# Kernel tuning notes

Measured on AMD Instinct MI355X. Metric: run time of the kernel, lower is better.

The kernel has to match this reference:

```python
import jax, jax.numpy as jnp
import numpy as np
import math

B, N, H, NH, L, NC = 8, 128, 128, 4, 4, 1
DH = H // NH
EPS = 1e-5

def _gelu(x):
    return jax.nn.gelu(x, approximate=False)  # torch nn.GELU default is exact erf

def _ln(x, g, b):
    m = x.mean(-1, keepdims=True)
    v = ((x - m) ** 2).mean(-1, keepdims=True)
    return (x - m) / jnp.sqrt(v + EPS) * g + b

def _bn(x, mask, g, b):
    # BatchNorm1d over valid (unpadded) nodes only, batch statistics (train mode)
    m = mask[..., None].astype(x.dtype)
    cnt = m.sum()
    mu = (x * m).sum((0, 1)) / cnt
    var = (((x - mu) ** 2) * m).sum((0, 1)) / cnt
    return (x - mu) / jnp.sqrt(var + EPS) * g + b

def _forward(e, u, atom_emb, bond_emb, eigw_W, eigw_b, mha_norm_g, mha_norm_b, qkv_W, qkv_b, out_W, out_b, ffn_norm_g, ffn_norm_b, ffn1_W, ffn1_b, ffn2_W, ffn2_b, dec_W, dec_b, fe1_W, fe1_b, fe2_W, fe2_b, pre_W, pre_b, f1_W, f1_b, bn1_g, bn1_b, f2_W, f2_b, bn2_g, bn2_b, lin_W, lin_b, node_feat, edge_feat, length):
    Bx, Nx = e.shape
    node_mask = jnp.arange(Nx)[None, :] < length[:, None]                        # [B,N]
    edge_mask = (node_mask[:, :, None] & node_mask[:, None, :]).astype(e.dtype)  # [B,src,dst]
    # SineEncoding
    div = jnp.exp(jnp.arange(0, H, 2, dtype=e.dtype) * (-math.log(10000.0) / H))
    pe = (e * 100.0)[:, :, None] * div
    eeig = jnp.concatenate([e[..., None], jnp.sin(pe), jnp.cos(pe)], axis=-1)    # [B,N,H+1]
    eig = eeig @ eigw_W.T + eigw_b                                               # [B,N,H]
    # multi-head self-attention over eigenvalue tokens with key padding mask
    xm = _ln(eig, mha_norm_g, mha_norm_b)
    qkv = xm @ qkv_W.T + qkv_b
    q, k, v = jnp.split(qkv, 3, axis=-1)
    q = q.reshape(Bx, Nx, NH, DH).transpose(0, 2, 1, 3)
    k = k.reshape(Bx, Nx, NH, DH).transpose(0, 2, 1, 3)
    v = v.reshape(Bx, Nx, NH, DH).transpose(0, 2, 1, 3)
    scores = jnp.einsum('bhqd,bhkd->bhqk', q, k) / math.sqrt(DH)
    scores = jnp.where(node_mask[:, None, None, :], scores, -jnp.inf)
    attn = jax.nn.softmax(scores, axis=-1)                                       # [B,NH,N,N]
    ctx = jnp.einsum('bhqk,bhkd->bhqd', attn, v).transpose(0, 2, 1, 3).reshape(Bx, Nx, H)
    eig = eig + (ctx @ out_W.T + out_b)
    y = _ln(eig, ffn_norm_g, ffn_norm_b)
    y = _gelu(y @ ffn1_W.T + ffn1_b) @ ffn2_W.T + ffn2_b
    eig = eig + y
    new_e = (eig @ dec_W.T + dec_b).transpose(0, 2, 1)                           # [B,NH,N]
    # spectral bases: identity + u @ diag(new_e_k) @ u^T per head, as fused diagonal scale
    filters = jnp.einsum('bnm,bkm,bpm->bnpk', u, new_e, u)                       # [B,N,N,NH]
    eye = jnp.broadcast_to(jnp.eye(Nx, dtype=e.dtype)[None, :, :, None], (Bx, Nx, Nx, 1))
    bases = jnp.concatenate([eye, filters], axis=-1)                             # [B,N,N,NH+1]
    bases = _gelu(_gelu(bases @ fe1_W.T + fe1_b) @ fe2_W.T + fe2_b)              # [B,N,N,H]
    xf = atom_emb[node_feat]                                                     # [B,N,H]
    ea = bond_emb[edge_feat]                                                     # [B,N,N,H]
    for l in range(L):
        # copy_u gather + per-edge FFN * bases + masked scatter-sum to dst
        msg = _gelu((xf[:, :, None, :] + ea) @ pre_W[l].T + pre_b[l]) * bases
        aggr = jnp.einsum('bijh,bij->bjh', msg, edge_mask)
        xf = xf + aggr
        y = xf @ f1_W[l].T + f1_b[l]
        y = jax.nn.relu(_bn(y, node_mask, bn1_g[l], bn1_b[l]))
        y = y @ f2_W[l].T + f2_b[l]
        y = jax.nn.relu(_bn(y, node_mask, bn2_g[l], bn2_b[l]))
        xf = xf + y
    nm = node_mask[..., None].astype(e.dtype)
    h = (xf * nm).sum(1) / length[:, None].astype(e.dtype)                       # AvgPooling over valid nodes
    h = h @ lin_W.T + lin_b
    return h, new_e, attn

def setup_inputs():
    key = jax.random.key(0)
    ks = iter(jax.random.split(key, 64))
    def w(*shape):
        return jax.random.normal(next(ks), shape, dtype=jnp.float32) * 0.02
    z = lambda *s: jnp.zeros(s, dtype=jnp.float32)
    o = lambda *s: jnp.ones(s, dtype=jnp.float32)
    e = jax.random.uniform(next(ks), (B, N), dtype=jnp.float32) * 2.0
    u = jnp.linalg.qr(jax.random.normal(next(ks), (B, N, N), dtype=jnp.float32))[0]
    inp = {
        'e': e, 'u': u,
        'atom_emb': w(40, H), 'bond_emb': w(10, H).at[0].set(0.0),
        'eigw_W': w(H, H + 1), 'eigw_b': z(H),
        'mha_norm_g': o(H), 'mha_norm_b': z(H),
        'qkv_W': w(3 * H, H), 'qkv_b': z(3 * H),
        'out_W': w(H, H), 'out_b': z(H),
        'ffn_norm_g': o(H), 'ffn_norm_b': z(H),
        'ffn1_W': w(H, H), 'ffn1_b': z(H),
        'ffn2_W': w(H, H), 'ffn2_b': z(H),
        'dec_W': w(NH, H), 'dec_b': z(NH),
        'fe1_W': w(H, NH + 1), 'fe1_b': z(H),
        'fe2_W': w(H, H), 'fe2_b': z(H),
        'pre_W': w(L, H, H), 'pre_b': z(L, H),
        'f1_W': w(L, H, H), 'f1_b': z(L, H),
        'bn1_g': o(L, H), 'bn1_b': z(L, H),
        'f2_W': w(L, H, H), 'f2_b': z(L, H),
        'bn2_g': o(L, H), 'bn2_b': z(L, H),
        'lin_W': w(NC, H), 'lin_b': z(NC),
        'node_feat': jax.random.randint(next(ks), (B, N), 0, 40),
        'edge_feat': jax.random.randint(next(ks), (B, N, N), 0, 10),
        'length': 64 + jax.random.randint(next(ks), (B,), 0, N - 63),
    }
    return inp

def reference(e, u, atom_emb, bond_emb, eigw_W, eigw_b, mha_norm_g, mha_norm_b, qkv_W, qkv_b, out_W, out_b, ffn_norm_g, ffn_norm_b, ffn1_W, ffn1_b, ffn2_W, ffn2_b, dec_W, dec_b, fe1_W, fe1_b, fe2_W, fe2_b, pre_W, pre_b, f1_W, f1_b, bn1_g, bn1_b, f2_W, f2_b, bn2_g, bn2_b, lin_W, lin_b, node_feat, edge_feat, length):
    return _forward(e, u, atom_emb, bond_emb, eigw_W, eigw_b, mha_norm_g, mha_norm_b, qkv_W, qkv_b, out_W, out_b, ffn_norm_g, ffn_norm_b, ffn1_W, ffn1_b, ffn2_W, ffn2_b, dec_W, dec_b, fe1_W, fe1_b, fe2_W, fe2_b, pre_W, pre_b, f1_W, f1_b, bn1_g, bn1_b, f2_W, f2_b, bn2_g, bn2_b, lin_W, lin_b, node_feat, edge_feat, length)
```

## Files before the change

kernel.cpp:

```cpp
#include <hip/hip_runtime.h>
#include <hip/hip_bf16.h>
#include <math.h>

#define BB 8
#define NN 128
#define HH 128
#define NHD 4
#define DHD 32
#define LAY 4
#define EPSV 1e-5f

typedef __hip_bfloat16 bf16;
typedef unsigned short ushortt;
typedef short bf16x8 __attribute__((ext_vector_type(8)));
typedef float f32x4 __attribute__((ext_vector_type(4)));

__device__ __forceinline__ float b2f(bf16 x){ return __bfloat162float(x); }
__device__ __forceinline__ bf16 f2b(float x){ return __float2bfloat16(x); }
__device__ __forceinline__ float us2f(ushortt u){ return __uint_as_float(((unsigned)u)<<16); }
__device__ __forceinline__ ushortt f2us(float x){ bf16 b=__float2bfloat16(x); return *(ushortt*)&b; }
__device__ __forceinline__ float gelu_f(float x){ return 0.5f*x*(1.0f+erff(x*0.7071067811865476f)); }
__device__ __forceinline__ float gelu_h(float x){
  float t = 0.7978845608028654f*x*(1.0f + 0.044715f*x*x);
  float e = __expf(2.0f*t);
  float th = 1.0f - 2.0f/(e + 1.0f);
  return 0.5f*x*(1.0f + th);
}
__device__ __forceinline__ float erf_fast(float x){
  float ax = fabsf(x);
  float t = __builtin_amdgcn_rcpf(__builtin_fmaf(0.3275911f, ax, 1.0f));
  float p = __builtin_fmaf(1.061405429f, t, -1.453152027f);
  p = __builtin_fmaf(p, t, 1.421413741f);
  p = __builtin_fmaf(p, t, -0.284496736f);
  p = __builtin_fmaf(p, t, 0.254829592f);
  p = p*t;
  float e = __expf(-ax*ax);
  float y = __builtin_fmaf(-p, e, 1.0f);
  return __builtin_copysignf(y, x);
}
__device__ __forceinline__ float gelu_fe(float x){
  return 0.5f*x*(1.0f + erf_fast(x*0.7071067811865476f));
}


__global__ __launch_bounds__(256) void k_prep(const float* __restrict__ fe2W,
    const float* __restrict__ preW, const float* __restrict__ eigW,
    const float* __restrict__ qkvW, const float* __restrict__ outW,
    const float* __restrict__ ffn1W, const float* __restrict__ ffn2W,
    const float* __restrict__ f1W, const float* __restrict__ f2W,
    const float* __restrict__ aemb, const int* __restrict__ nf,
    const float* __restrict__ bemb, const float* __restrict__ preb,
    ushortt* __restrict__ wbf, float* __restrict__ gs, float* __restrict__ xf0,
    float* __restrict__ eigWT, float* __restrict__ qkvWT, float* __restrict__ outWT,
    float* __restrict__ ffn1WT, float* __restrict__ ffn2WT,
    float* __restrict__ f1WT, float* __restrict__ f2WT,
    float* __restrict__ bondWall){
  int idx = blockIdx.x*256 + threadIdx.x;
  if (idx < 10240) gs[idx] = 0.f;
  if (idx < 81920){
    float v = (idx < 16384) ? fe2W[idx] : preW[idx - 16384];
    wbf[idx] = f2us(v);
  }
  if (idx < 131072){
    int node = idx >> 7, h2 = idx & 127;
    xf0[idx] = aemb[nf[node]*HH + h2];
  }
  if (idx < 16512){ int o = idx/129, kq = idx - o*129; eigWT[kq*128+o] = eigW[idx]; }
  if (idx < 49152){ int o = idx>>7, m = idx&127; qkvWT[m*384+o] = qkvW[idx]; }
  if (idx < 16384){ int o = idx>>7, m = idx&127;
    outWT[m*128+o]  = outW[idx];
    ffn1WT[m*128+o] = ffn1W[idx];
    ffn2WT[m*128+o] = ffn2W[idx];
  }
  if (idx < 65536){ int l = idx>>14, r = idx&16383; int o = r>>7, m = r&127;
    f1WT[l*16384 + m*128+o] = f1W[idx];
    f2WT[l*16384 + m*128+o] = f2W[idx];
  }
  if (idx < 5120){
    int l = idx / 1280; int r = idx - l*1280; int e2 = r >> 7; int hcol = r & 127;
    const float* br = bemb + e2*128;
    const float* wr = preW + l*16384 + hcol*128;
    float acc = preb[l*128 + hcol];
    for (int m=0;m<128;m++) acc += br[m]*wr[m];
    bondWall[idx] = acc;
  }
}


__global__ void k_fe_a(const float* __restrict__ e, const float* __restrict__ eigWT,
                       const float* __restrict__ eigb, const float* __restrict__ g,
                       const float* __restrict__ bt, const float* __restrict__ qkvWT,
                       const float* __restrict__ qkvb,
                       float* __restrict__ eigout, float* __restrict__ q,
                       float* __restrict__ kT, float* __restrict__ v){
  int row = blockIdx.x; int tid = threadIdx.x;
  int b = row >> 7, n = row & 127;
  __shared__ float ee[129]; __shared__ float buf[128]; __shared__ float xm[128];
  float ev = e[row];
  if (tid < 64){
    float dv = expf(-0.1439115683121279f * (float)tid);
    float pe = ev * 100.0f * dv;
    ee[1+tid] = sinf(pe);
    ee[65+tid] = cosf(pe);
  }
  if (tid == 0) ee[0] = ev;
  __syncthreads();
  float x = eigb[tid];
  for (int k2=0;k2<129;k2++) x += ee[k2]*eigWT[k2*128+tid];
  eigout[row*HH+tid] = x;
  buf[tid]=x; __syncthreads();
  for (int s2=64;s2>0;s2>>=1){ if(tid<s2) buf[tid]+=buf[tid+s2]; __syncthreads(); }
  float mean = buf[0]*(1.0f/128.0f); __syncthreads();
  float d = x-mean; buf[tid]=d*d; __syncthreads();
  for (int s2=64;s2>0;s2>>=1){ if(tid<s2) buf[tid]+=buf[tid+s2]; __syncthreads(); }
  float var = buf[0]*(1.0f/128.0f);
  xm[tid] = d*rsqrtf(var+EPSV)*g[tid]+bt[tid];
  __syncthreads();
  #pragma unroll
  for (int s3=0;s3<3;s3++){
    float acc = qkvb[s3*HH+tid];
    const float* wt = qkvWT + s3*HH + tid;
    for (int m=0;m<HH;m++) acc += xm[m]*wt[m*384];
    if (s3==0) q[row*HH+tid]=acc;
    else if (s3==1) kT[b*16384 + tid*128 + n]=acc;
    else v[row*HH+tid]=acc;
  }
}

__global__ void k_attn(const float* __restrict__ q, const float* __restrict__ kT,
                       const int* __restrict__ length,
                       float* __restrict__ attnf, float* __restrict__ outp){
  int bx = blockIdx.x;
  int qi = bx & 127, hd = (bx>>7)&3, b = bx>>9;
  int tid = threadIdx.x;
  int len = length[b];
  __shared__ float qv[DHD]; __shared__ float red[128];
  if (tid < DHD) qv[tid] = q[(b*NN+qi)*HH + hd*DHD + tid];
  __syncthreads();
  float s = -1e30f;
  if (tid < len){
    const float* kr = kT + b*16384 + hd*DHD*128 + tid;
    float sc=0.f;
    for (int d2=0; d2<DHD; d2++) sc += qv[d2]*kr[d2*128];
    s = sc * 0.17677669529663687f;
  }
  red[tid]=s; __syncthreads();
  for (int st=64;st>0;st>>=1){ if(tid<st) red[tid]=fmaxf(red[tid],red[tid+st]); __syncthreads(); }
  float mx = red[0]; __syncthreads();
  float p = (tid<len)? expf(s-mx):0.0f;
  red[tid]=p; __syncthreads();
  for (int st=64;st>0;st>>=1){ if(tid<st) red[tid]+=red[tid+st]; __syncthreads(); }
  float a = p / red[0];
  int idx = ((b*NHD+hd)*NN+qi)*NN+tid;
  attnf[idx]=a;
  outp[4104 + idx]=a;
}

__global__ void k_fe_c(const float* __restrict__ attnf, const float* __restrict__ v,
                       const float* __restrict__ outWT, const float* __restrict__ outb,
                       const float* __restrict__ fng, const float* __restrict__ fnb,
                       const float* __restrict__ w1T, const float* __restrict__ b1,
                       const float* __restrict__ w2T, const float* __restrict__ b2,
                       float* __restrict__ eig){
  int row = blockIdx.x; int b = row>>7, qi = row&127;
  int tid = threadIdx.x;
  __shared__ float c[128]; __shared__ float buf[128]; __shared__ float xm[128]; __shared__ float tt[128];
  int hd = tid>>5;
  const float* ar = attnf + ((b*NHD+hd)*NN+qi)*NN;
  float acc=0.f;
  for (int j=0;j<NN;j++) acc += ar[j]*v[(b*NN+j)*HH+tid];
  c[tid]=acc; __syncthreads();
  float o = outb[tid];
  for (int m=0;m<HH;m++) o += c[m]*outWT[m*128+tid];
  float x = eig[row*HH+tid] + o;
  buf[tid]=x; __syncthreads();
  for (int s2=64;s2>0;s2>>=1){ if(tid<s2) buf[tid]+=buf[tid+s2]; __syncthreads(); }
  float mean=buf[0]*(1.f/128.f); __syncthreads();
  float d=x-mean; buf[tid]=d*d; __syncthreads();
  for (int s2=64;s2>0;s2>>=1){ if(tid<s2) buf[tid]+=buf[tid+s2]; __syncthreads(); }
  float var=buf[0]*(1.f/128.f);
  xm[tid]=d*rsqrtf(var+EPSV)*fng[tid]+fnb[tid];
  __syncthreads();
  float a1=b1[tid];
  for (int m=0;m<HH;m++) a1+=xm[m]*w1T[m*128+tid];
  tt[tid]=gelu_f(a1); __syncthreads();
  float a2=b2[tid];
  for (int m=0;m<HH;m++) a2+=tt[m]*w2T[m*128+tid];
  eig[row*HH+tid]=x+a2;
}

__global__ void k_dec(const float* __restrict__ eig, const float* dW, const float* db,
                      float* __restrict__ newe, float* __restrict__ outp){
  int b = blockIdx.x, n = threadIdx.x;
  __shared__ float w[NHD*HH];
  for (int i=n;i<NHD*HH;i+=128) w[i]=dW[i];
  __syncthreads();
  float acc[NHD];
  #pragma unroll
  for (int kk=0;kk<NHD;kk++) acc[kk]=db[kk];
  const float* er = eig + (b*NN+n)*HH;
  for (int h2=0;h2<HH;h2++){
    float ev = er[h2];
    #pragma unroll
    for (int kk=0;kk<NHD;kk++) acc[kk]+=ev*w[kk*HH+h2];
  }
  #pragma unroll
  for (int kk=0;kk<NHD;kk++){
    int idx=(b*NHD+kk)*NN+n; newe[idx]=acc[kk];
    outp[8 + idx]=acc[kk];
  }
}


__global__ void k_filters(const float* __restrict__ u, const float* __restrict__ newe,
                          const int* __restrict__ length, float* __restrict__ filt){
  int b = blockIdx.x, n0 = blockIdx.y*16, p0 = blockIdx.z*16;
  int len = length[b];
  if (n0 >= len || p0 >= len) return;
  int tx = threadIdx.x, ty = threadIdx.y; int tid = ty*16+tx;
  __shared__ float un[16][17], upt[16][17], wk[4][16];
  float acc[4]={0.f,0.f,0.f,0.f};
  for (int mt=0; mt<8; mt++){
    __syncthreads();
    un[ty][tx]  = u[(b*NN+n0+ty)*NN + mt*16+tx];
    upt[tx][ty] = u[(b*NN+p0+ty)*NN + mt*16+tx];
    if (tid<64) wk[tid>>4][tid&15] = newe[(b*NHD+(tid>>4))*NN + mt*16 + (tid&15)];
    __syncthreads();
    #pragma unroll
    for (int mm=0;mm<16;mm++){
      float pr = un[ty][mm]*upt[mm][tx];
      #pragma unroll
      for (int kk=0;kk<4;kk++) acc[kk] += pr*wk[kk][mm];
    }
  }
  float4 o; o.x=acc[0];o.y=acc[1];o.z=acc[2];o.w=acc[3];
  *(float4*)&filt[((b*NN+n0+ty)*NN+p0+tx)*4] = o;
}

__global__ __launch_bounds__(256) void k_fe2(const float* __restrict__ filt,
    const float* __restrict__ w1g, const float* __restrict__ b1g,
    const ushortt* __restrict__ w2bf, const float* __restrict__ b2g,
    const int* __restrict__ length,
    bf16* __restrict__ bases){
  int blk = blockIdx.x;
  int bi = blk >> 1;
  int r0 = (blk & 1)*64;
  int b = bi >> 7;
  int nloc = bi & 127;
  int len = length[b];
  if (nloc >= len || r0 >= len) return;
  int tid = threadIdx.x;
  int lane = tid & 63, w = tid >> 6, quad = lane >> 4, l15 = lane & 15;
  int pr = r0 + w*16 + l15;
  float4 f4 = ((const float4*)filt)[bi*128 + pr];
  __shared__ alignas(16) ushortt sW2[128*136];
  __shared__ float w1p[128*8];
  __shared__ float b2s[128];
  for (int idx = tid; idx < 2048; idx += 256){
    int r = idx >> 4, cb = idx & 15;
    *(uint4*)&sW2[r*136 + cb*8] = *(const uint4*)&w2bf[r*128 + cb*8];
  }
  for (int idx = tid; idx < 1024; idx += 256){
    int r = idx >> 3, c = idx & 7;
    w1p[idx] = (c==0) ? b1g[r] : (c<=5 ? w1g[r*5 + c-1] : 0.f);
  }
  if (tid < 128) b2s[tid] = b2g[tid];
  __syncthreads();
  bool wact = (r0 + w*16) < len;
  f32x4 acc[8];
  #pragma unroll
  for (int nt=0;nt<8;nt++) acc[nt] = (f32x4){0.f,0.f,0.f,0.f};
  if (wact){
    float dg = (pr == nloc) ? 1.0f : 0.0f;
    for (int kk = 0; kk < 128; kk += 32){
      bf16x8 af;
      #pragma unroll
      for (int j=0;j<8;j++){
        int m = kk + quad*8 + j;
        const float4 wa = *(const float4*)&w1p[m*8];
        const float2 wb = *(const float2*)&w1p[m*8+4];
        float a = wa.x + wa.y*dg + wa.z*f4.x + wa.w*f4.y + wb.x*f4.z + wb.y*f4.w;
        af[j] = (short)f2us(gelu_fe(a));
      }
      #pragma unroll
      for (int nt=0;nt<8;nt++){
        bf16x8 bfr = *(const bf16x8*)&sW2[(nt*16+l15)*136 + kk + quad*8];
        acc[nt] = __builtin_amdgcn_mfma_f32_16x16x32_bf16(af, bfr, acc[nt], 0, 0, 0);
      }
    }
  }
  __syncthreads();
  ushortt* sT = sW2;
  if (wact){
    #pragma unroll
    for (int nt=0;nt<8;nt++){
      int h = nt*16 + l15;
      float bb = b2s[h];
      #pragma unroll
      for (int reg=0;reg<4;reg++){
        int lr = w*16 + quad*4 + reg;
        sT[lr*132 + h] = f2us(gelu_fe(acc[nt][reg] + bb));
      }
    }
  }
  __syncthreads();
  int rmax = len - r0; if (rmax > 64) rmax = 64;
  ushort4* gout = (ushort4*)(bases + (size_t)bi*16384 + r0*128);
  for (int idx = tid; idx < rmax*32; idx += 256){
    int row = idx >> 5, seg = idx & 31;
    gout[idx] = *(const ushort4*)&sT[row*132 + seg*4];
  }
}


__global__ __launch_bounds__(256) void k_xwl2(const float* __restrict__ xfprev,
    const float* __restrict__ t2, const float* __restrict__ gsum2p,
    const float* __restrict__ gsq2p, const float* __restrict__ g2p,
    const float* __restrict__ bb2p, const int* __restrict__ length, int prevapply,
    const ushortt* __restrict__ wbfl, float* __restrict__ xfB,
    float* __restrict__ xfW){
  int blk = blockIdx.x;
  int b = blk >> 2, rq = blk & 3;
  int tid = threadIdx.x;
  int lane = tid & 63, w = tid >> 6, quad = lane >> 4, l15 = lane & 15;
  __shared__ alignas(16) ushortt sA[32*136];
  __shared__ float smu[128], sistd[128], sg[128], sbb[128];
  if (prevapply && tid < 128){
    float cnt = 0.f;
    for (int q2=0;q2<BB;q2++) cnt += (float)length[q2];
    float mu = gsum2p[tid]/cnt;
    float var = gsq2p[tid]/cnt - mu*mu;
    smu[tid]=mu; sistd[tid]=rsqrtf(fmaxf(var,0.0f)+EPSV);
    sg[tid]=g2p[tid]; sbb[tid]=bb2p[tid];
  }
  __syncthreads();
  for (int idx = tid; idx < 1024; idx += 256){
    int r = idx >> 5, c = idx & 31;
    int gr = b*128 + rq*32 + r;
    float4 xv = ((const float4*)xfprev)[gr*32 + c];
    if (prevapply){
      float4 tv = ((const float4*)t2)[gr*32 + c];
      int f0 = c*4;
      xv.x += fmaxf((tv.x-smu[f0+0])*sistd[f0+0]*sg[f0+0]+sbb[f0+0], 0.f);
      xv.y += fmaxf((tv.y-smu[f0+1])*sistd[f0+1]*sg[f0+1]+sbb[f0+1], 0.f);
      xv.z += fmaxf((tv.z-smu[f0+2])*sistd[f0+2]*sg[f0+2]+sbb[f0+2], 0.f);
      xv.w += fmaxf((tv.w-smu[f0+3])*sistd[f0+3]*sg[f0+3]+sbb[f0+3], 0.f);
      ((float4*)xfB)[gr*32 + c] = xv;
    }
    ushort4 o;
    o.x=f2us(xv.x); o.y=f2us(xv.y); o.z=f2us(xv.z); o.w=f2us(xv.w);
    *(ushort4*)&sA[r*136 + c*4] = o;
  }
  __syncthreads();
  f32x4 acc[2][2];
  #pragma unroll
  for (int mt=0;mt<2;mt++)
    #pragma unroll
    for (int nt=0;nt<2;nt++) acc[mt][nt] = (f32x4){0.f,0.f,0.f,0.f};
  #pragma unroll
  for (int kk = 0; kk < 128; kk += 32){
    bf16x8 af[2], bfr[2];
    #pragma unroll
    for (int mt=0;mt<2;mt++) af[mt] = *(const bf16x8*)&sA[(mt*16+l15)*136 + kk + quad*8];
    #pragma unroll
    for (int nt=0;nt<2;nt++) bfr[nt] = *(const bf16x8*)&wbfl[((w*2+nt)*16+l15)*128 + kk + quad*8];
    #pragma unroll
    for (int mt=0;mt<2;mt++)
      #pragma unroll
      for (int nt=0;nt<2;nt++)
        acc[mt][nt] = __builtin_amdgcn_mfma_f32_16x16x32_bf16(af[mt], bfr[nt], acc[mt][nt], 0, 0, 0);
  }
  #pragma unroll
  for (int mt=0;mt<2;mt++)
    #pragma unroll
    for (int nt=0;nt<2;nt++){
      int h = (w*2+nt)*16 + l15;
      #pragma unroll
      for (int reg=0;reg<4;reg++){
        int prr = rq*32 + mt*16 + quad*4 + reg;
        xfW[(b*128 + prr)*128 + h] = acc[mt][nt][reg];
      }
    }
}

__global__ __launch_bounds__(512) void k_edge(const float* __restrict__ xfin, float* __restrict__ xfout,
    const bf16* __restrict__ bases, const float* __restrict__ xfW,
    const float* __restrict__ bondWl, const int* __restrict__ ef,
    const int* __restrict__ length,
    const float* __restrict__ w1t, const float* __restrict__ bias1,
    float* __restrict__ t1, float* __restrict__ gst){
  int bj = blockIdx.x; int b = bj >> 7, j = bj & 127;
  int len = length[b];
  int tid = threadIdx.x; int h = tid & 127, ih = tid >> 7;
  __shared__ float sBW[10][128];
  __shared__ int sEf[128];
  __shared__ float part[4][128];
  for (int idx = tid; idx < 1280; idx += 512) sBW[idx>>7][idx&127] = bondWl[idx];
  if (tid < 128) sEf[tid] = ef[(b*NN + tid)*NN + j];
  __syncthreads();
  float agg = 0.f;
  if (j < len){
    const float* xwb = xfW + b*NN*HH + h;
    const bf16* bb = bases + ((size_t)b*NN + j)*NN*HH + h;
    for (int i = ih; i < len; i += 4){
      float vv = gelu_h(xwb[i*128] + sBW[sEf[i]][h]);
      agg += vv * b2f(bb[i*128]);
    }
  }
  part[ih][h] = agg; __syncthreads();
  if (tid < 128){
    int o = (b*NN + j)*HH + tid;
    float xrow = xfin[o] + part[0][tid] + part[1][tid] + part[2][tid] + part[3][tid];
    xfout[o] = xrow;
    part[0][tid] = xrow;
  }
  __syncthreads();
  float acc = (ih==0) ? bias1[h] : 0.f;
  {
    const float* wcol = w1t + h;
    int m0 = ih*32;
    for (int m = m0; m < m0+32; m++) acc += part[0][m]*wcol[m*128];
  }
  float* red = &sBW[0][0];
  __syncthreads();
  red[ih*128 + h] = acc; __syncthreads();
  if (tid < 128){
    float t1v = red[tid] + red[128+tid] + red[256+tid] + red[384+tid];
    t1[(b*NN + j)*HH + tid] = t1v;
    if (j < len){
      int bank = bj & 7;
      atomicAdd(&gst[bank*256 + tid], t1v);
      atomicAdd(&gst[bank*256 + 128 + tid], t1v*t1v);
    }
  }
}

__global__ __launch_bounds__(256) void k_g2s(const float* __restrict__ t1,
    const float* __restrict__ gstL,
    const float* __restrict__ g1, const float* __restrict__ bb1,
    const float* __restrict__ w2t, const float* __restrict__ bias2,
    const int* __restrict__ length, float* __restrict__ t2){
  int blk = blockIdx.x; int tid = threadIdx.x;
  int f = tid & 127, rh = tid >> 7;
  __shared__ float sy[4][128];
  __shared__ float red1[2][128], red2[2][128];
  int r0 = blk*4;
  float cnt = 0.f;
  for (int b=0;b<BB;b++) cnt += (float)length[b];
  float su = 0.f, sq = 0.f;
  #pragma unroll
  for (int k=0;k<8;k++){ su += gstL[k*256 + f]; sq += gstL[k*256 + 128 + f]; }
  float mu = su/cnt;
  float var = sq/cnt - mu*mu;
  float istd = rsqrtf(fmaxf(var,0.0f)+EPSV);
  float gg = g1[f], bbv = bb1[f];
  for (int idx = tid; idx < 512; idx += 256){
    int r = idx >> 7;
    float x = t1[(r0+r)*128 + f];
    float y = (x-mu)*istd*gg + bbv;
    sy[r][f] = fmaxf(y, 0.0f);
  }
  __syncthreads();
  float bsv = bias2[f];
  float s=0.f, s2=0.f;
  for (int rr = rh*2; rr < rh*2+2; rr++){
    int rg = r0 + rr; int b = rg >> 7, n = rg & 127;
    float acc = bsv;
    for (int m=0;m<128;m++) acc += sy[rr][m]*w2t[m*128+f];
    t2[rg*128+f] = acc;
    if (n < length[b]){ s += acc; s2 += acc*acc; }
  }
  red1[rh][f]=s; red2[rh][f]=s2; __syncthreads();
  if (tid < 128){
    atomicAdd((float*)&gstL[2048 + tid], red1[0][tid]+red1[1][tid]);
    atomicAdd((float*)&gstL[2048 + 128 + tid], red2[0][tid]+red2[1][tid]);
  }
}

__global__ void k_pool2(const float* __restrict__ xf, const float* __restrict__ t2,
                        const float* __restrict__ gsum2, const float* __restrict__ gsq2,
                        const float* __restrict__ g2, const float* __restrict__ bb2,
                        const int* __restrict__ length,
                        const float* lw, const float* lb, float* __restrict__ outp){
  int b = blockIdx.x, tid=threadIdx.x;
  int len = length[b];
  float cnt = 0.f;
  for (int q2=0;q2<BB;q2++) cnt += (float)length[q2];
  float mu = gsum2[tid]/cnt;
  float var = gsq2[tid]/cnt - mu*mu;
  float istd = rsqrtf(fmaxf(var,0.0f)+EPSV);
  float gg = g2[tid], bbv = bb2[tid];
  float s=0.f;
  for (int n2=0;n2<len;n2++){
    int o = (b*NN+n2)*HH+tid;
    float x = xf[o] + fmaxf((t2[o]-mu)*istd*gg+bbv, 0.0f);
    s += x;
  }
  s /= (float)len;
  __shared__ float red[128];
  red[tid]=s*lw[tid]; __syncthreads();
  for (int st=64;st>0;st>>=1){ if(tid<st) red[tid]+=red[tid+st]; __syncthreads(); }
  if (tid==0) outp[b]=red[0]+lb[0];
}


extern "C" void kernel_launch(void* const* d_in, const int* in_sizes, int n_in,
                              void* d_out, int out_size, void* d_ws, size_t ws_size,
                              hipStream_t stream) {
  (void)in_sizes; (void)n_in; (void)out_size; (void)ws_size;
  const float* e        = (const float*)d_in[0];
  const float* u        = (const float*)d_in[1];
  const float* atom_emb = (const float*)d_in[2];
  const float* bond_emb = (const float*)d_in[3];
  const float* eigw_W   = (const float*)d_in[4];
  const float* eigw_b   = (const float*)d_in[5];
  const float* mng      = (const float*)d_in[6];
  const float* mnb      = (const float*)d_in[7];
  const float* qkvW     = (const float*)d_in[8];
  const float* qkvb     = (const float*)d_in[9];
  const float* outW     = (const float*)d_in[10];
  const float* outb     = (const float*)d_in[11];
  const float* fng      = (const float*)d_in[12];
  const float* fnb      = (const float*)d_in[13];
  const float* ffn1W    = (const float*)d_in[14];
  const float* ffn1b    = (const float*)d_in[15];
  const float* ffn2W    = (const float*)d_in[16];
  const float* ffn2b    = (const float*)d_in[17];
  const float* decW     = (const float*)d_in[18];
  const float* decb     = (const float*)d_in[19];
  const float* fe1W     = (const float*)d_in[20];
  const float* fe1b     = (const float*)d_in[21];
  const float* fe2W     = (const float*)d_in[22];
  const float* fe2b     = (const float*)d_in[23];
  const float* preW     = (const float*)d_in[24];
  const float* preb     = (const float*)d_in[25];
  const float* f1W      = (const float*)d_in[26];
  const float* f1b      = (const float*)d_in[27];
  const float* bn1g     = (const float*)d_in[28];
  const float* bn1b     = (const float*)d_in[29];
  const float* f2W      = (const float*)d_in[30];
  const float* f2b      = (const float*)d_in[31];
  const float* bn2g     = (const float*)d_in[32];
  const float* bn2b     = (const float*)d_in[33];
  const float* linW     = (const float*)d_in[34];
  const float* linb     = (const float*)d_in[35];
  const int* nodef      = (const int*)d_in[36];
  const int* edgef      = (const int*)d_in[37];
  const int* length     = (const int*)d_in[38];

  float* outp = (float*)d_out;

  char* p = (char*)d_ws;
  auto alloc = [&](size_t bytes)->void*{ void* r=(void*)p; p += (bytes+255)&~(size_t)255; return r; };
  const int TOK = BB*NN*HH;
  float* eig   = (float*)alloc(TOK*4);
  float* q     = (float*)alloc(TOK*4);
  float* kT    = (float*)alloc(TOK*4);
  float* v     = (float*)alloc(TOK*4);
  float* attnf = (float*)alloc((size_t)BB*NHD*NN*NN*4);
  float* newe  = (float*)alloc(BB*NHD*NN*4);
  float* filt  = (float*)alloc((size_t)BB*NN*NN*4*4);
  bf16*  bases = (bf16*) alloc((size_t)BB*NN*NN*HH*2);
  float* xf0   = (float*)alloc(TOK*4);
  float* xfB   = (float*)alloc(TOK*4);
  float* xfC   = (float*)alloc(TOK*4);
  float* xfD   = (float*)alloc(TOK*4);
  float* t1    = (float*)alloc(TOK*4);
  float* t2    = (float*)alloc(TOK*4);
  float* xfW   = (float*)alloc(TOK*4);
  float* gs    = (float*)alloc(10240*4);
  ushortt* wbf = (ushortt*)alloc(81920*2);
  float* eigWT = (float*)alloc(16512*4);
  float* qkvWT = (float*)alloc(49152*4);
  float* outWT = (float*)alloc(16384*4);
  float* ffn1WT= (float*)alloc(16384*4);
  float* ffn2WT= (float*)alloc(16384*4);
  float* f1WT  = (float*)alloc(65536*4);
  float* f2WT  = (float*)alloc(65536*4);
  float* bondWall = (float*)alloc(5120*4);

  k_prep<<<512, 256, 0, stream>>>(fe2W, preW, eigw_W, qkvW, outW, ffn1W, ffn2W,
                                  f1W, f2W, atom_emb, nodef, bond_emb, preb,
                                  wbf, gs, xf0, eigWT, qkvWT, outWT, ffn1WT,
                                  ffn2WT, f1WT, f2WT, bondWall);

  k_fe_a<<<BB*NN, 128, 0, stream>>>(e, eigWT, eigw_b, mng, mnb, qkvWT, qkvb, eig, q, kT, v);
  k_attn<<<BB*NHD*NN, 128, 0, stream>>>(q, kT, length, attnf, outp);
  k_fe_c<<<BB*NN, 128, 0, stream>>>(attnf, v, outWT, outb, fng, fnb,
                                    ffn1WT, ffn1b, ffn2WT, ffn2b, eig);
  k_dec<<<BB, 128, 0, stream>>>(eig, decW, decb, newe, outp);

  k_filters<<<dim3(BB,8,8), dim3(16,16), 0, stream>>>(u, newe, length, filt);
  k_fe2<<<2*BB*NN, 256, 0, stream>>>(filt, fe1W, fe1b, wbf, fe2b, length, bases);

  const float* xfprev = xf0;
  float* xfcur = xfC;
  for (int l=0;l<LAY;l++){
    const ushortt* wbfl = wbf + 16384 + l*16384;
    float* gsl = gs + l*2560;
    float* gsp = gs + (l-1)*2560;
    k_xwl2<<<BB*4, 256, 0, stream>>>(xfprev, t2,
                                   (l>0)? gsp+2048 : gs, (l>0)? gsp+2048+128 : gs,
                                   bn2g + (l>0? (l-1)*HH:0), bn2b + (l>0? (l-1)*HH:0),
                                   length, (l>0)?1:0,
                                   wbfl, xfB, xfW);
    const float* xin = (l==0)? xf0 : xfB;
    k_edge<<<BB*NN, 512, 0, stream>>>(xin, xfcur, bases, xfW, bondWall + l*1280,
                                      edgef, length,
                                      f1WT + l*16384, f1b + l*HH, t1, gsl);
    k_g2s<<<256, 256, 0, stream>>>(t1, gsl, bn1g + l*HH, bn1b + l*HH,
                                   f2WT + l*16384, f2b + l*HH, length, t2);
    xfprev = xfcur;
    xfcur = (xfcur == xfC) ? xfD : xfC;
  }
  k_pool2<<<BB, 128, 0, stream>>>(xfprev, t2, gs+3*2560+2048, gs+3*2560+2048+128,
                                  bn2g + 3*HH, bn2b + 3*HH, length, linW, linb, outp);
}
```

Baseline: 413.4 us.

## Fuse attention, FFN, and decoder into one kernel; compute filters inside fe2

Measured after the change: 409.9 us. No clear change (-0.9%).

```diff
diff --git a/kernel.cpp b/kernel.cpp
--- a/kernel.cpp
+++ b/kernel.cpp
@@ -17,7 +17,6 @@
 
 __device__ __forceinline__ float b2f(bf16 x){ return __bfloat162float(x); }
 __device__ __forceinline__ bf16 f2b(float x){ return __float2bfloat16(x); }
-__device__ __forceinline__ float us2f(ushortt u){ return __uint_as_float(((unsigned)u)<<16); }
 __device__ __forceinline__ ushortt f2us(float x){ bf16 b=__float2bfloat16(x); return *(ushortt*)&b; }
 __device__ __forceinline__ float gelu_f(float x){ return 0.5f*x*(1.0f+erff(x*0.7071067811865476f)); }
 __device__ __forceinline__ float gelu_h(float x){
@@ -127,117 +126,90 @@
   }
 }
 
-__global__ void k_attn(const float* __restrict__ q, const float* __restrict__ kT,
-                       const int* __restrict__ length,
-                       float* __restrict__ attnf, float* __restrict__ outp){
-  int bx = blockIdx.x;
-  int qi = bx & 127, hd = (bx>>7)&3, b = bx>>9;
-  int tid = threadIdx.x;
-  int len = length[b];
-  __shared__ float qv[DHD]; __shared__ float red[128];
-  if (tid < DHD) qv[tid] = q[(b*NN+qi)*HH + hd*DHD + tid];
-  __syncthreads();
-  float s = -1e30f;
-  if (tid < len){
-    const float* kr = kT + b*16384 + hd*DHD*128 + tid;
-    float sc=0.f;
-    for (int d2=0; d2<DHD; d2++) sc += qv[d2]*kr[d2*128];
-    s = sc * 0.17677669529663687f;
-  }
-  red[tid]=s; __syncthreads();
-  for (int st=64;st>0;st>>=1){ if(tid<st) red[tid]=fmaxf(red[tid],red[tid+st]); __syncthreads(); }
-  float mx = red[0]; __syncthreads();
-  float p = (tid<len)? expf(s-mx):0.0f;
-  red[tid]=p; __syncthreads();
-  for (int st=64;st>0;st>>=1){ if(tid<st) red[tid]+=red[tid+st]; __syncthreads(); }
-  float a = p / red[0];
-  int idx = ((b*NHD+hd)*NN+qi)*NN+tid;
-  attnf[idx]=a;
-  outp[4104 + idx]=a;
-}
-
-__global__ void k_fe_c(const float* __restrict__ attnf, const float* __restrict__ v,
-                       const float* __restrict__ outWT, const float* __restrict__ outb,
-                       const float* __restrict__ fng, const float* __restrict__ fnb,
-                       const float* __restrict__ w1T, const float* __restrict__ b1,
-                       const float* __restrict__ w2T, const float* __restrict__ b2,
-                       float* __restrict__ eig){
+__global__ __launch_bounds__(512) void k_attc(const float* __restrict__ q,
+    const float* __restrict__ kT, const float* __restrict__ v,
+    const float* __restrict__ eig, const int* __restrict__ length,
+    const float* __restrict__ outWT, const float* __restrict__ outb,
+    const float* __restrict__ fng, const float* __restrict__ fnb,
+    const float* __restrict__ w1T, const float* __restrict__ b1,
+    const float* __restrict__ w2T, const float* __restrict__ b2,
+    const float* __restrict__ dW, const float* __restrict__ db,
+    float* __restrict__ newe, float* __restrict__ outp){
   int row = blockIdx.x; int b = row>>7, qi = row&127;
   int tid = threadIdx.x;
-  __shared__ float c[128]; __shared__ float buf[128]; __shared__ float xm[128]; __shared__ float tt[128];
-  int hd = tid>>5;
-  const float* ar = attnf + ((b*NHD+hd)*NN+qi)*NN;
-  float acc=0.f;
-  for (int j=0;j<NN;j++) acc += ar[j]*v[(b*NN+j)*HH+tid];
-  c[tid]=acc; __syncthreads();
-  float o = outb[tid];
-  for (int m=0;m<HH;m++) o += c[m]*outWT[m*128+tid];
-  float x = eig[row*HH+tid] + o;
-  buf[tid]=x; __syncthreads();
-  for (int s2=64;s2>0;s2>>=1){ if(tid<s2) buf[tid]+=buf[tid+s2]; __syncthreads(); }
-  float mean=buf[0]*(1.f/128.f); __syncthreads();
-  float d=x-mean; buf[tid]=d*d; __syncthreads();
-  for (int s2=64;s2>0;s2>>=1){ if(tid<s2) buf[tid]+=buf[tid+s2]; __syncthreads(); }
-  float var=buf[0]*(1.f/128.f);
-  xm[tid]=d*rsqrtf(var+EPSV)*fng[tid]+fnb[tid];
-  __syncthreads();
-  float a1=b1[tid];
-  for (int m=0;m<HH;m++) a1+=xm[m]*w1T[m*128+tid];
-  tt[tid]=gelu_f(a1); __syncthreads();
-  float a2=b2[tid];
-  for (int m=0;m<HH;m++) a2+=tt[m]*w2T[m*128+tid];
-  eig[row*HH+tid]=x+a2;
-}
-
-__global__ void k_dec(const float* __restrict__ eig, const float* dW, const float* db,
-                      float* __restrict__ newe, float* __restrict__ outp){
-  int b = blockIdx.x, n = threadIdx.x;
-  __shared__ float w[NHD*HH];
-  for (int i=n;i<NHD*HH;i+=128) w[i]=dW[i];
-  __syncthreads();
-  float acc[NHD];
-  #pragma unroll
-  for (int kk=0;kk<NHD;kk++) acc[kk]=db[kk];
-  const float* er = eig + (b*NN+n)*HH;
-  for (int h2=0;h2<HH;h2++){
-    float ev = er[h2];
-    #pragma unroll
-    for (int kk=0;kk<NHD;kk++) acc[kk]+=ev*w[kk*HH+h2];
-  }
-  #pragma unroll
-  for (int kk=0;kk<NHD;kk++){
-    int idx=(b*NHD+kk)*NN+n; newe[idx]=acc[kk];
-    outp[8 + idx]=acc[kk];
-  }
-}
-
-
-__global__ void k_filters(const float* __restrict__ u, const float* __restrict__ newe,
-                          const int* __restrict__ length, float* __restrict__ filt){
-  int b = blockIdx.x, n0 = blockIdx.y*16, p0 = blockIdx.z*16;
+  int hg = tid>>7, lt = tid&127;
   int len = length[b];
-  if (n0 >= len || p0 >= len) return;
-  int tx = threadIdx.x, ty = threadIdx.y; int tid = ty*16+tx;
-  __shared__ float un[16][17], upt[16][17], wk[4][16];
-  float acc[4]={0.f,0.f,0.f,0.f};
-  for (int mt=0; mt<8; mt++){
-    __syncthreads();
-    un[ty][tx]  = u[(b*NN+n0+ty)*NN + mt*16+tx];
-    upt[tx][ty] = u[(b*NN+p0+ty)*NN + mt*16+tx];
-    if (tid<64) wk[tid>>4][tid&15] = newe[(b*NHD+(tid>>4))*NN + mt*16 + (tid&15)];
-    __syncthreads();
-    #pragma unroll
-    for (int mm=0;mm<16;mm++){
-      float pr = un[ty][mm]*upt[mm][tx];
-      #pragma unroll
-      for (int kk=0;kk<4;kk++) acc[kk] += pr*wk[kk][mm];
-    }
-  }
-  float4 o; o.x=acc[0];o.y=acc[1];o.z=acc[2];o.w=acc[3];
-  *(float4*)&filt[((b*NN+n0+ty)*NN+p0+tx)*4] = o;
-}
-
-__global__ __launch_bounds__(256) void k_fe2(const float* __restrict__ filt,
+  __shared__ float qv[4][DHD];
+  __shared__ float red[4][128];
+  __shared__ float satt[4][128];
+  __shared__ float sc[128], sbuf[128], sxm[128], stt[128], sx[128];
+  if (lt < DHD) qv[hg][lt] = q[(b*NN+qi)*HH + hg*DHD + lt];
+  __syncthreads();
+  float s = -1e30f;
+  if (lt < len){
+    const float* kr = kT + b*16384 + hg*DHD*128 + lt;
+    float scr=0.f;
+    for (int d2=0; d2<DHD; d2++) scr += qv[hg][d2]*kr[d2*128];
+    s = scr * 0.17677669529663687f;
+  }
+  red[hg][lt]=s; __syncthreads();
+  for (int st=64;st>0;st>>=1){ if(lt<st) red[hg][lt]=fmaxf(red[hg][lt],red[hg][lt+st]); __syncthreads(); }
+  float mx = red[hg][0]; __syncthreads();
+  float pp = (lt<len)? expf(s-mx):0.0f;
+  red[hg][lt]=pp; __syncthreads();
+  for (int st=64;st>0;st>>=1){ if(lt<st) red[hg][lt]+=red[hg][lt+st]; __syncthreads(); }
+  float a = pp / red[hg][0];
+  satt[hg][lt] = a;
+  outp[4104 + ((b*NHD+hg)*NN+qi)*NN + lt] = a;
+  __syncthreads();
+  if (tid < 128){
+    int hd = tid>>5;
+    float acc=0.f;
+    for (int j=0;j<NN;j++) acc += satt[hd][j]*v[(b*NN+j)*HH+tid];
+    sc[tid]=acc;
+  }
+  __syncthreads();
+  if (tid < 128){
+    float o = outb[tid];
+    for (int m=0;m<HH;m++) o += sc[m]*outWT[m*128+tid];
+    float x = eig[row*HH+tid] + o;
+    sx[tid] = x; sbuf[tid] = x;
+  }
+  __syncthreads();
+  for (int s2=64;s2>0;s2>>=1){ if(tid<s2) sbuf[tid]+=sbuf[tid+s2]; __syncthreads(); }
+  float mean = sbuf[0]*(1.f/128.f); __syncthreads();
+  if (tid < 128){ float d = sx[tid]-mean; sbuf[tid]=d*d; }
+  __syncthreads();
+  for (int s2=64;s2>0;s2>>=1){ if(tid<s2) sbuf[tid]+=sbuf[tid+s2]; __syncthreads(); }
+  float var = sbuf[0]*(1.f/128.f);
+  if (tid < 128){
+    float d = sx[tid]-mean;
+    sxm[tid] = d*rsqrtf(var+EPSV)*fng[tid]+fnb[tid];
+  }
+  __syncthreads();
+  if (tid < 128){
+    float a1=b1[tid];
+    for (int m=0;m<HH;m++) a1+=sxm[m]*w1T[m*128+tid];
+    stt[tid]=gelu_f(a1);
+  }
+  __syncthreads();
+  if (tid < 128){
+    float a2=b2[tid];
+    for (int m=0;m<HH;m++) a2+=stt[m]*w2T[m*128+tid];
+    sx[tid] = sx[tid] + a2;
+  }
+  __syncthreads();
+  if (tid < 4){
+    float acc = db[tid];
+    const float* wr = dW + tid*HH;
+    for (int h2=0;h2<HH;h2++) acc += sx[h2]*wr[h2];
+    int idx=(b*NHD+tid)*NN+qi;
+    newe[idx]=acc; outp[8+idx]=acc;
+  }
+}
+
+__global__ __launch_bounds__(256) void k_fe2(const float* __restrict__ u,
+    const float* __restrict__ newe,
     const float* __restrict__ w1g, const float* __restrict__ b1g,
     const ushortt* __restrict__ w2bf, const float* __restrict__ b2g,
     const int* __restrict__ length,
@@ -252,10 +224,10 @@
   int tid = threadIdx.x;
   int lane = tid & 63, w = tid >> 6, quad = lane >> 4, l15 = lane & 15;
   int pr = r0 + w*16 + l15;
-  float4 f4 = ((const float4*)filt)[bi*128 + pr];
   __shared__ alignas(16) ushortt sW2[128*136];
   __shared__ float w1p[128*8];
   __shared__ float b2s[128];
+  __shared__ float cn[4][128];
   for (int idx = tid; idx < 2048; idx += 256){
     int r = idx >> 4, cb = idx & 15;
     *(uint4*)&sW2[r*136 + cb*8] = *(const uint4*)&w2bf[r*128 + cb*8];
@@ -263,6 +235,10 @@
   for (int idx = tid; idx < 1024; idx += 256){
     int r = idx >> 3, c = idx & 7;
     w1p[idx] = (c==0) ? b1g[r] : (c<=5 ? w1g[r*5 + c-1] : 0.f);
+  }
+  for (int idx = tid; idx < 512; idx += 256){
+    int k = idx >> 7, m = idx & 127;
+    cn[k][m] = u[(b*NN+nloc)*NN + m] * newe[(b*NHD+k)*NN + m];
   }
   if (tid < 128) b2s[tid] = b2g[tid];
   __syncthreads();
@@ -271,6 +247,16 @@
   #pragma unroll
   for (int nt=0;nt<8;nt++) acc[nt] = (f32x4){0.f,0.f,0.f,0.f};
   if (wact){
+    float f0=0.f, f1=0.f, f2v=0.f, f3=0.f;
+    const float4* ur = (const float4*)(u + ((size_t)b*NN + pr)*NN);
+    for (int m4 = 0; m4 < 32; m4++){
+      float4 uv = ur[m4];
+      int m = m4*4;
+      f0 += cn[0][m]*uv.x; f0 += cn[0][m+1]*uv.y; f0 += cn[0][m+2]*uv.z; f0 += cn[0][m+3]*uv.w;
+      f1 += cn[1][m]*uv.x; f1 += cn[1][m+1]*uv.y; f1 += cn[1][m+2]*uv.z; f1 += cn[1][m+3]*uv.w;
+      f2v += cn[2][m]*uv.x; f2v += cn[2][m+1]*uv.y; f2v += cn[2][m+2]*uv.z; f2v += cn[2][m+3]*uv.w;
+      f3 += cn[3][m]*uv.x; f3 += cn[3][m+1]*uv.y; f3 += cn[3][m+2]*uv.z; f3 += cn[3][m+3]*uv.w;
+    }
     float dg = (pr == nloc) ? 1.0f : 0.0f;
     for (int kk = 0; kk < 128; kk += 32){
       bf16x8 af;
@@ -279,7 +265,7 @@
         int m = kk + quad*8 + j;
         const float4 wa = *(const float4*)&w1p[m*8];
         const float2 wb = *(const float2*)&w1p[m*8+4];
-        float a = wa.x + wa.y*dg + wa.z*f4.x + wa.w*f4.y + wb.x*f4.z + wb.y*f4.w;
+        float a = wa.x + wa.y*dg + wa.z*f0 + wa.w*f1 + wb.x*f2v + wb.y*f3;
         af[j] = (short)f2us(gelu_fe(a));
       }
       #pragma unroll
@@ -557,9 +543,7 @@
   float* q     = (float*)alloc(TOK*4);
   float* kT    = (float*)alloc(TOK*4);
   float* v     = (float*)alloc(TOK*4);
-  float* attnf = (float*)alloc((size_t)BB*NHD*NN*NN*4);
   float* newe  = (float*)alloc(BB*NHD*NN*4);
-  float* filt  = (float*)alloc((size_t)BB*NN*NN*4*4);
   bf16*  bases = (bf16*) alloc((size_t)BB*NN*NN*HH*2);
   float* xf0   = (float*)alloc(TOK*4);
   float* xfB   = (float*)alloc(TOK*4);
@@ -585,13 +569,12 @@
                                   ffn2WT, f1WT, f2WT, bondWall);
 
   k_fe_a<<<BB*NN, 128, 0, stream>>>(e, eigWT, eigw_b, mng, mnb, qkvWT, qkvb, eig, q, kT, v);
-  k_attn<<<BB*NHD*NN, 128, 0, stream>>>(q, kT, length, attnf, outp);
-  k_fe_c<<<BB*NN, 128, 0, stream>>>(attnf, v, outWT, outb, fng, fnb,
-                                    ffn1WT, ffn1b, ffn2WT, ffn2b, eig);
-  k_dec<<<BB, 128, 0, stream>>>(eig, decW, decb, newe, outp);
-
-  k_filters<<<dim3(BB,8,8), dim3(16,16), 0, stream>>>(u, newe, length, filt);
-  k_fe2<<<2*BB*NN, 256, 0, stream>>>(filt, fe1W, fe1b, wbf, fe2b, length, bases);
+  k_attc<<<BB*NN, 512, 0, stream>>>(q, kT, v, eig, length,
+                                    outWT, outb, fng, fnb,
+                                    ffn1WT, ffn1b, ffn2WT, ffn2b,
+                                    decW, decb, newe, outp);
+
+  k_fe2<<<2*BB*NN, 256, 0, stream>>>(u, newe, fe1W, fe1b, wbf, fe2b, length, bases);
 
   const float* xfprev = xf0;
   float* xfcur = xfC;
```
